# Kernel tuning notes

Hardware: AMD Instinct MI355X
Metric: run time of the kernel (lower is better)

## Reference

```python
import jax, jax.numpy as jnp
import numpy as np

B, P, D, H, DH = 2, 2048, 1024, 16, 64
EPS = 1e-5

def layernorm(x, g, b):
    mu = jnp.mean(x, axis=-1, keepdims=True)
    var = jnp.mean((x - mu) ** 2, axis=-1, keepdims=True)
    return (x - mu) * jax.lax.rsqrt(var + EPS) * g + b

def setup_inputs() -> dict:
    key = jax.random.key(0)
    ks = jax.random.split(key, 16)
    s = lambda *sh: 1.0 / np.sqrt(sh[-2] if len(sh) > 1 else sh[-1])
    return {
        "x": jax.random.normal(ks[0], (B, P, D), jnp.float32),
        "Wq": jax.random.normal(ks[1], (H, D, DH), jnp.float32) / np.sqrt(D),
        "Wk": jax.random.normal(ks[2], (H, D, DH), jnp.float32) / np.sqrt(D),
        "Wv": jax.random.normal(ks[3], (H, D, DH), jnp.float32) / np.sqrt(D),
        "Wp": jax.random.normal(ks[4], (D, D), jnp.float32) / np.sqrt(D),
        "bp": jax.random.normal(ks[5], (D,), jnp.float32) * 0.01,
        "W1": jax.random.normal(ks[6], (D, 4 * D), jnp.float32) / np.sqrt(D),
        "b1": jax.random.normal(ks[7], (4 * D,), jnp.float32) * 0.01,
        "W2": jax.random.normal(ks[8], (4 * D, D), jnp.float32) / np.sqrt(4 * D),
        "b2": jax.random.normal(ks[9], (D,), jnp.float32) * 0.01,
        "g1": jnp.ones((D,), jnp.float32),
        "be1": jnp.zeros((D,), jnp.float32),
        "g2": jnp.ones((D,), jnp.float32),
        "be2": jnp.zeros((D,), jnp.float32),
    }

def reference(x, Wq, Wk, Wv, Wp, bp, W1, b1, W2, b2, g1, be1, g2, be2):
    Bb, Pp, Dd = x.shape
    h = layernorm(x, g1, be1)
    # per-head projections, stacked: [B,H,P,DH]
    q = jnp.einsum('bpd,hde->bhpe', h, Wq)
    k = jnp.einsum('bpd,hde->bhpe', h, Wk)
    v = jnp.einsum('bpd,hde->bhpe', h, Wv)
    # NOTE: source scales by dim_embd**-0.5 (C = x.shape[-1]), not dim_head
    scores = jnp.einsum('bhpe,bhqe->bhpq', q, k) * (Dd ** -0.5)
    mask = jnp.tril(jnp.ones((Pp, Pp), bool))
    scores = jnp.where(mask, scores, -jnp.inf)
    att = jax.nn.softmax(scores, axis=-1)
    o = jnp.einsum('bhpq,bhqe->bhpe', att, v)
    # concat heads: [B,P,H*DH]
    o = o.transpose(0, 2, 1, 3).reshape(Bb, Pp, -1)
    x = x + o @ Wp + bp
    h2 = layernorm(x, g2, be2)
    m = jax.nn.gelu(h2 @ W1 + b1, approximate=False)
    x = x + m @ W2 + b2
    return x
```

## Files before the change

### kernel.cpp

```cpp
#include <hip/hip_runtime.h>
#include <hip/hip_bf16.h>
#include <stdint.h>

typedef unsigned short u16;
typedef __attribute__((ext_vector_type(4))) float f32x4;
typedef __attribute__((ext_vector_type(8))) short bf16x8;
typedef __attribute__((ext_vector_type(4))) short bf16x4;
typedef __attribute__((ext_vector_type(4))) unsigned short u16x4;

static __device__ __forceinline__ u16 f2bf(float f) {
    union { float f; unsigned u; } v; v.f = f;
    unsigned r = v.u + 0x7fffu + ((v.u >> 16) & 1u);
    return (u16)(r >> 16);
}

static __device__ __forceinline__ void gload_lds16(const u16* g, u16* l) {
    __builtin_amdgcn_global_load_lds(
        (const __attribute__((address_space(1))) void*)(uintptr_t)g,
        (__attribute__((address_space(3))) void*)(uint32_t)(uintptr_t)l,
        16, 0, 0);
}

__global__ __launch_bounds__(256) void transpose_cast_b(
    const float* __restrict__ W, u16* __restrict__ out,
    int K, int N, long in_bs, long out_bs)
{
    __shared__ float tile[32][33];
    const float* Wb = W + (size_t)blockIdx.z * in_bs;
    u16* ob = out + (size_t)blockIdx.z * out_bs;
    int nt = blockIdx.x * 32, kt = blockIdx.y * 32;
    int tx = threadIdx.x & 31, ty = threadIdx.x >> 5;
    #pragma unroll
    for (int i = ty; i < 32; i += 8)
        tile[i][tx] = Wb[(size_t)(kt + i) * N + nt + tx];
    __syncthreads();
    #pragma unroll
    for (int i = ty; i < 32; i += 8)
        ob[(size_t)(nt + i) * K + kt + tx] = f2bf(tile[tx][i]);
}

__global__ __launch_bounds__(256) void ln_kernel(
    const float* __restrict__ x, const float* __restrict__ g,
    const float* __restrict__ be, u16* __restrict__ out)
{
    int row = blockIdx.x;
    int t = threadIdx.x;
    const float4* xr = (const float4*)(x + (size_t)row * 1024);
    float4 v = xr[t];
    float s = v.x + v.y + v.z + v.w;
    float sq = v.x * v.x + v.y * v.y + v.z * v.z + v.w * v.w;
    #pragma unroll
    for (int o = 1; o < 64; o <<= 1) {
        s  += __shfl_xor(s, o);
        sq += __shfl_xor(sq, o);
    }
    __shared__ float ps[4], pq[4];
    if ((t & 63) == 0) { ps[t >> 6] = s; pq[t >> 6] = sq; }
    __syncthreads();
    float S = ps[0] + ps[1] + ps[2] + ps[3];
    float Q = pq[0] + pq[1] + pq[2] + pq[3];
    float mu = S * (1.0f / 1024.0f);
    float var = Q * (1.0f / 1024.0f) - mu * mu;
    float rs = rsqrtf(var + 1e-5f);
    const float4 g4  = ((const float4*)g)[t];
    const float4 be4 = ((const float4*)be)[t];
    u16x4 o4;
    o4[0] = f2bf((v.x - mu) * rs * g4.x + be4.x);
    o4[1] = f2bf((v.y - mu) * rs * g4.y + be4.y);
    o4[2] = f2bf((v.z - mu) * rs * g4.z + be4.z);
    o4[3] = f2bf((v.w - mu) * rs * g4.w + be4.w);
    *(u16x4*)(out + (size_t)row * 1024 + t * 4) = o4;
}

template<int EPI>
__global__ __launch_bounds__(256) void gemm_bt(
    const u16* __restrict__ A, const u16* __restrict__ Bt,
    int M, int N, int K,
    const float* __restrict__ bias,
    void* __restrict__ Cout, u16* __restrict__ Kf, u16* __restrict__ Vf)
{
    __shared__ __align__(16) u16 SH[32768];
    const int tm = blockIdx.y * 128, tn = blockIdx.x * 128;
    const int t = threadIdx.x;
    const int lane = t & 63, wave = t >> 6;
    const int wr = wave >> 1, wc = wave & 1;
    const int lq = lane & 15, lg = lane >> 4;
    f32x4 acc[4][4] = {};

    const int srow8 = lane >> 3;
    const int skoff = ((lane & 7) ^ srow8) * 8;
    const u16* ag = A  + (size_t)(tm + wave * 32 + srow8) * K + skoff;
    const u16* bg = Bt + (size_t)(tn + wave * 32 + srow8) * K + skoff;

    auto STAGE = [&](int buf, int k0) {
        u16* ab = SH + buf * 16384 + wave * 2048;
        u16* bb = SH + buf * 16384 + 8192 + wave * 2048;
        #pragma unroll
        for (int j = 0; j < 4; ++j) {
            gload_lds16(ag + (size_t)(j * 8) * K + k0, ab + j * 512);
            gload_lds16(bg + (size_t)(j * 8) * K + k0, bb + j * 512);
        }
    };

    const int KT = K >> 6;
    STAGE(0, 0);
    __syncthreads();
    int buf = 0;
    for (int kt = 0; kt < KT; ++kt) {
        if (kt + 1 < KT) STAGE(buf ^ 1, (kt + 1) << 6);
        const u16* abuf = SH + buf * 16384;
        const u16* bbuf = abuf + 8192;
        bf16x8 af[4][2], bfv[4][2];
        #pragma unroll
        for (int m = 0; m < 4; ++m) {
            const int row = wr * 64 + m * 16 + lq;
            #pragma unroll
            for (int kk = 0; kk < 2; ++kk) {
                const int slot = (kk * 4 + lg) ^ (row & 7);
                af[m][kk] = *(const bf16x8*)(abuf + row * 64 + slot * 8);
            }
        }
        #pragma unroll
        for (int n = 0; n < 4; ++n) {
            const int col = wc * 64 + n * 16 + lq;
            #pragma unroll
            for (int kk = 0; kk < 2; ++kk) {
                const int slot = (kk * 4 + lg) ^ (col & 7);
                bfv[n][kk] = *(const bf16x8*)(bbuf + col * 64 + slot * 8);
            }
        }
        #pragma unroll
        for (int m = 0; m < 4; ++m)
            #pragma unroll
            for (int n = 0; n < 4; ++n)
                #pragma unroll
                for (int kk = 0; kk < 2; ++kk)
                    acc[m][n] = __builtin_amdgcn_mfma_f32_16x16x32_bf16(
                        af[m][kk], bfv[n][kk], acc[m][n], 0, 0, 0);
        __syncthreads();
        buf ^= 1;
    }

    if (EPI == 2 || (EPI == 3 && tn < 1024)) {
        #pragma unroll
        for (int n = 0; n < 4; ++n) {
            const int cl = wc * 64 + n * 16 + lq;
            #pragma unroll
            for (int m = 0; m < 4; ++m) {
                const int rl = wr * 64 + m * 16 + lg * 4;
                #pragma unroll
                for (int r = 0; r < 4; ++r) {
                    float v = acc[m][n][r];
                    if (EPI == 2) {
                        float xx = v + bias[tn + cl];
                        v = 0.5f * xx * (1.0f + erff(xx * 0.70710678118654752f));
                    }
                    SH[(rl + r) * 136 + cl] = f2bf(v);
                }
            }
        }
        __syncthreads();
        const int row = t >> 1, half = t & 1;
        const int ncols = (EPI == 2) ? N : 1024;
        const uint4* srow4 = (const uint4*)(SH + row * 136 + half * 64);
        uint4* drow = (uint4*)((u16*)Cout + (size_t)(tm + row) * ncols + tn + half * 64);
        #pragma unroll
        for (int i = 0; i < 8; ++i)
            drow[i] = srow4[i];
    } else if (EPI == 3) {
        const bool isK = (tn < 2048);
        #pragma unroll
        for (int n = 0; n < 4; ++n) {
            const int cl = wc * 64 + n * 16 + lq;
            const int d = cl & 63, hl = cl >> 6;
            #pragma unroll
            for (int m = 0; m < 4; ++m) {
                const int rl0 = wr * 64 + m * 16 + lg * 4;
                #pragma unroll
                for (int r = 0; r < 4; ++r) {
                    const int rl = rl0 + r;
                    const int p = rl & 63, kl = rl >> 6;
                    int off;
                    if (isK)
                        off = ((p >> 4) * 2 + (d >> 5)) * 512 + ((d >> 3) & 3) * 128
                            + (p & 15) * 8 + (d & 7);
                    else
                        off = ((p >> 4) * 4 + (d >> 4)) * 256 + ((p >> 2) & 3) * 64
                            + (d & 15) * 4 + (p & 3);
                    SH[(hl * 2 + kl) * 4096 + off] = f2bf(acc[m][n][r]);
                }
            }
        }
        __syncthreads();
        const int img = t >> 6, ln = t & 63;
        const int hl = img >> 1, kl = img & 1;
        const int hh = ((tn - (isK ? 1024 : 2048)) >> 6) + hl;
        const int bb = tm >> 11, pp = tm & 2047;
        u16* base = (isK ? Kf : Vf) + (size_t)(bb * 16 + hh) * 131072
                  + (size_t)((pp >> 6) + kl) * 4096;
        const u16* simg = SH + img * 4096;
        #pragma unroll
        for (int i = 0; i < 8; ++i)
            *(uint4*)(base + ln * 8 + i * 512) = *(const uint4*)(simg + ln * 8 + i * 512);
    }
}

__global__ __launch_bounds__(256) void gemm_bt64(
    const u16* __restrict__ A, const u16* __restrict__ Bt,
    int M, int N, int K,
    const float* __restrict__ bias, const float* __restrict__ res,
    float* __restrict__ Cout)
{
    __shared__ __align__(16) u16 As[128 * 32];
    __shared__ __align__(16) u16 Bs[64 * 32];
    const int tm = blockIdx.y * 128, tn = blockIdx.x * 64;
    const int t = threadIdx.x;
    const int lane = t & 63, wave = t >> 6;
    const int wr = wave >> 1, wc = wave & 1;
    const int lq = lane & 15, lg = lane >> 4;
    f32x4 acc[4][2] = {};
    const int srow  = wave * 32 + (lane >> 2);
    const int srowB = wave * 16 + (lane >> 2);
    const int scol = (lane & 3) * 8;
    const u16* ag = A  + (size_t)(tm + srow)  * K + scol;
    const u16* bg = Bt + (size_t)(tn + srowB) * K + scol;
    u16* asl = As + wave * 1024;
    u16* bsl = Bs + wave * 512;
    const size_t rowskip = (size_t)16 * K;
    for (int k0 = 0; k0 < K; k0 += 32) {
        gload_lds16(ag + k0,           asl);
        gload_lds16(ag + k0 + rowskip, asl + 512);
        gload_lds16(bg + k0,           bsl);
        __syncthreads();
        bf16x8 af[4], bfr[2];
        #pragma unroll
        for (int m = 0; m < 4; ++m)
            af[m] = *(const bf16x8*)(As + (wr * 64 + m * 16 + lq) * 32 + lg * 8);
        #pragma unroll
        for (int n = 0; n < 2; ++n)
            bfr[n] = *(const bf16x8*)(Bs + (wc * 32 + n * 16 + lq) * 32 + lg * 8);
        #pragma unroll
        for (int m = 0; m < 4; ++m)
            #pragma unroll
            for (int n = 0; n < 2; ++n)
                acc[m][n] = __builtin_amdgcn_mfma_f32_16x16x32_bf16(af[m], bfr[n], acc[m][n], 0, 0, 0);
        __syncthreads();
    }
    #pragma unroll
    for (int m = 0; m < 4; ++m)
        #pragma unroll
        for (int n = 0; n < 2; ++n) {
            const int col = tn + wc * 32 + n * 16 + lq;
            #pragma unroll
            for (int r = 0; r < 4; ++r) {
                const int row = tm + wr * 64 + m * 16 + lg * 4 + r;
                Cout[(size_t)row * N + col] = acc[m][n][r] + bias[col] + res[(size_t)row * N + col];
            }
        }
}

__global__ __launch_bounds__(256, 4) void attn_kernel(
    const u16* __restrict__ qb, const u16* __restrict__ Kf,
    const u16* __restrict__ Vf, u16* __restrict__ o)
{
    const int P = 2048;
    __shared__ __align__(16) u16 KB[2][4096];
    __shared__ __align__(16) u16 VB[2][4096];
    int blk = blockIdx.x;
    int qt = 31 - (blk >> 5);
    int bh = blk & 31;
    int h = bh & 15, b = bh >> 4;
    int w = threadIdx.x >> 6, lane = threadIdx.x & 63;
    int lq = lane & 15, lg = lane >> 4;
    int q0 = qt * 64 + w * 16;
    const u16* qptr = qb + (size_t)(b * P + q0 + lq) * 1024 + h * 64 + lg * 8;
    bf16x8 qf0 = *(const bf16x8*)qptr;
    bf16x8 qf1 = *(const bf16x8*)(qptr + 32);
    const u16* Kfb = Kf + (size_t)bh * 131072;
    const u16* Vfb = Vf + (size_t)bh * 131072;
    const float C2 = 0.03125f * 1.44269504f;
    const int moff = w * 16 + lq;
    float m2 = -1e30f, l_run = 0.f;
    f32x4 accO[4] = {};
    const int nkvb = qt + 1;

    const int vsel = w >> 1, half = w & 1;
    auto STAGE = [&](int buf, int kvb) {
        const u16* src = (vsel ? Vfb : Kfb) + (size_t)kvb * 4096 + half * 2048 + lane * 8;
        u16* dst = (vsel ? &VB[buf][half * 2048] : &KB[buf][half * 2048]);
        #pragma unroll
        for (int i = 0; i < 4; ++i)
            gload_lds16(src + i * 512, dst + i * 512);
    };

    auto COMPUTE = [&](int buf, bool last) {
        const u16* kbase = KB[buf] + lane * 8;
        f32x4 st[4];
        #pragma unroll
        for (int ss = 0; ss < 4; ++ss) {
            bf16x8 kf0 = *(const bf16x8*)(kbase + ss * 1024);
            bf16x8 kf1 = *(const bf16x8*)(kbase + ss * 1024 + 512);
            f32x4 z = {0.f, 0.f, 0.f, 0.f};
            st[ss] = __builtin_amdgcn_mfma_f32_16x16x32_bf16(kf0, qf0, z, 0, 0, 0);
            st[ss] = __builtin_amdgcn_mfma_f32_16x16x32_bf16(kf1, qf1, st[ss], 0, 0, 0);
        }
        float rmax = -1e30f;
        #pragma unroll
        for (int ss = 0; ss < 4; ++ss)
            #pragma unroll
            for (int r = 0; r < 4; ++r) {
                float v = st[ss][r] * C2;
                if (last && (ss * 16 + lg * 4 + r > moff)) v = -1e30f;
                st[ss][r] = v;
                rmax = fmaxf(rmax, v);
            }
        rmax = fmaxf(rmax, __shfl_xor(rmax, 16));
        rmax = fmaxf(rmax, __shfl_xor(rmax, 32));
        if (__any(rmax > m2 + 11.5f)) {
            float m2n = fmaxf(m2, rmax);
            float alpha = exp2f(m2 - m2n);
            l_run *= alpha;
            #pragma unroll
            for (int r = 0; r < 4; ++r) {
                float ar = __shfl(alpha, lg * 4 + r);
                accO[0][r] *= ar; accO[1][r] *= ar; accO[2][r] *= ar; accO[3][r] *= ar;
            }
            m2 = m2n;
        }
        float psum = 0.f;
        bf16x4 pf[4];
        #pragma unroll
        for (int ss = 0; ss < 4; ++ss)
            #pragma unroll
            for (int r = 0; r < 4; ++r) {
                float pv = exp2f(st[ss][r] - m2);
                psum += pv;
                pf[ss][r] = (short)f2bf(pv);
            }
        psum += __shfl_xor(psum, 16);
        psum += __shfl_xor(psum, 32);
        l_run += psum;
        const u16* vbase = VB[buf] + lane * 4;
        #pragma unroll
        for (int ks = 0; ks < 4; ++ks)
            #pragma unroll
            for (int c = 0; c < 4; ++c) {
                bf16x4 vfr = *(const bf16x4*)(vbase + (ks * 4 + c) * 256);
                accO[c] = __builtin_amdgcn_mfma_f32_16x16x16bf16_1k(pf[ks], vfr, accO[c], 0, 0, 0);
            }
    };

    STAGE(0, 0);
    __syncthreads();
    int cur = 0;
    for (int kvb = 0; kvb < nkvb; ++kvb) {
        if (kvb + 1 < nkvb) STAGE(cur ^ 1, kvb + 1);
        COMPUTE(cur, kvb == nkvb - 1);
        __syncthreads();
        cur ^= 1;
    }

    #pragma unroll
    for (int r = 0; r < 4; ++r) {
        float l_r = __shfl(l_run, lg * 4 + r);
        float inv = 1.0f / l_r;
        size_t orow = (size_t)(b * P + q0 + lg * 4 + r) * 1024 + h * 64;
        #pragma unroll
        for (int c = 0; c < 4; ++c)
            o[orow + c * 16 + lq] = f2bf(accO[c][r] * inv);
    }
}

extern "C" void kernel_launch(void* const* d_in, const int* in_sizes, int n_in,
                              void* d_out, int out_size, void* d_ws, size_t ws_size,
                              hipStream_t stream)
{
    const float* x   = (const float*)d_in[0];
    const float* Wq  = (const float*)d_in[1];
    const float* Wk  = (const float*)d_in[2];
    const float* Wv  = (const float*)d_in[3];
    const float* Wp  = (const float*)d_in[4];
    const float* bp  = (const float*)d_in[5];
    const float* W1  = (const float*)d_in[6];
    const float* b1  = (const float*)d_in[7];
    const float* W2  = (const float*)d_in[8];
    const float* b2  = (const float*)d_in[9];
    const float* g1  = (const float*)d_in[10];
    const float* be1 = (const float*)d_in[11];
    const float* g2  = (const float*)d_in[12];
    const float* be2 = (const float*)d_in[13];

    char* ws = (char*)d_ws;
    u16*  h     = (u16*)(ws + 0);
    u16*  qbuf  = (u16*)(ws + 8388608);
    u16*  Kf    = (u16*)(ws + 16777216);
    u16*  Vf    = (u16*)(ws + 25165824);
    u16*  o     = (u16*)(ws + 33554432);
    float* x1   = (float*)(ws + 41943040);
    u16*  wqkvT = (u16*)(ws + 58720256);
    u16*  wpT   = (u16*)(ws + 65011712);
    u16*  w1T   = (u16*)(ws + 67108864);
    u16*  w2T   = (u16*)(ws + 75497472);
    u16*  m     = (u16*)(ws + 0);
    u16*  h2    = o;
    float* out  = (float*)d_out;

    transpose_cast_b<<<dim3(2, 32, 16), 256, 0, stream>>>(Wq, wqkvT,           1024, 64, 65536, 65536);
    transpose_cast_b<<<dim3(2, 32, 16), 256, 0, stream>>>(Wk, wqkvT + 1048576, 1024, 64, 65536, 65536);
    transpose_cast_b<<<dim3(2, 32, 16), 256, 0, stream>>>(Wv, wqkvT + 2097152, 1024, 64, 65536, 65536);
    transpose_cast_b<<<dim3(32, 32, 1), 256, 0, stream>>>(Wp, wpT, 1024, 1024, 0, 0);
    transpose_cast_b<<<dim3(128, 32, 1), 256, 0, stream>>>(W1, w1T, 1024, 4096, 0, 0);
    transpose_cast_b<<<dim3(32, 128, 1), 256, 0, stream>>>(W2, w2T, 4096, 1024, 0, 0);

    ln_kernel<<<4096, 256, 0, stream>>>(x, g1, be1, h);
    gemm_bt<3><<<dim3(24, 32), 256, 0, stream>>>(h, wqkvT, 4096, 3072, 1024, nullptr, qbuf, Kf, Vf);
    attn_kernel<<<1024, 256, 0, stream>>>(qbuf, Kf, Vf, o);
    gemm_bt64<<<dim3(16, 32), 256, 0, stream>>>(o, wpT, 4096, 1024, 1024, bp, x, x1);
    ln_kernel<<<4096, 256, 0, stream>>>(x1, g2, be2, h2);
    gemm_bt<2><<<dim3(32, 32), 256, 0, stream>>>(h2, w1T, 4096, 4096, 1024, b1, m, nullptr, nullptr);
    gemm_bt64<<<dim3(16, 32), 256, 0, stream>>>(m, w2T, 4096, 1024, 4096, b2, x1, out);
}
```

Measured before the change: 278.2 us.

## Enlarge bf16 GEMM tiles to 256x256 with 512-thread blocks

The QKV and FFN1 GEMMs move from 128x128 tiles with 4 waves to 256x256 tiles with 8 waves, each wave computing 128x64. This doubles the LDS buffer to 128KB and reuses each A fragment across four MFMAs to raise arithmetic intensity per staged byte. The epilogues are rewritten to write the output in two row halves, and the K/V image layout is adapted to the larger tile. It risks lower occupancy (one block per CU), fewer blocks than CUs (192 and 256 blocks), and higher register pressure.

```diff
diff --git a/kernel.cpp b/kernel.cpp
--- a/kernel.cpp
+++ b/kernel.cpp
@@ -73,19 +73,19 @@
 }
 
 template<int EPI>
-__global__ __launch_bounds__(256) void gemm_bt(
+__global__ __launch_bounds__(512, 1) void gemm256(
     const u16* __restrict__ A, const u16* __restrict__ Bt,
     int M, int N, int K,
     const float* __restrict__ bias,
     void* __restrict__ Cout, u16* __restrict__ Kf, u16* __restrict__ Vf)
 {
-    __shared__ __align__(16) u16 SH[32768];
-    const int tm = blockIdx.y * 128, tn = blockIdx.x * 128;
+    __shared__ __align__(16) u16 SH[65536];
+    const int tm = blockIdx.y * 256, tn = blockIdx.x * 256;
     const int t = threadIdx.x;
     const int lane = t & 63, wave = t >> 6;
-    const int wr = wave >> 1, wc = wave & 1;
+    const int wm = wave >> 2, wn = wave & 3;
     const int lq = lane & 15, lg = lane >> 4;
-    f32x4 acc[4][4] = {};
+    f32x4 acc[8][4] = {};
 
     const int srow8 = lane >> 3;
     const int skoff = ((lane & 7) ^ srow8) * 8;
@@ -93,8 +93,8 @@
     const u16* bg = Bt + (size_t)(tn + wave * 32 + srow8) * K + skoff;
 
     auto STAGE = [&](int buf, int k0) {
-        u16* ab = SH + buf * 16384 + wave * 2048;
-        u16* bb = SH + buf * 16384 + 8192 + wave * 2048;
+        u16* ab = SH + buf * 32768 + wave * 2048;
+        u16* bb = SH + buf * 32768 + 16384 + wave * 2048;
         #pragma unroll
         for (int j = 0; j < 4; ++j) {
             gload_lds16(ag + (size_t)(j * 8) * K + k0, ab + j * 512);
@@ -108,21 +108,12 @@
     int buf = 0;
     for (int kt = 0; kt < KT; ++kt) {
         if (kt + 1 < KT) STAGE(buf ^ 1, (kt + 1) << 6);
-        const u16* abuf = SH + buf * 16384;
-        const u16* bbuf = abuf + 8192;
-        bf16x8 af[4][2], bfv[4][2];
-        #pragma unroll
-        for (int m = 0; m < 4; ++m) {
-            const int row = wr * 64 + m * 16 + lq;
-            #pragma unroll
-            for (int kk = 0; kk < 2; ++kk) {
-                const int slot = (kk * 4 + lg) ^ (row & 7);
-                af[m][kk] = *(const bf16x8*)(abuf + row * 64 + slot * 8);
-            }
-        }
+        const u16* abuf = SH + buf * 32768;
+        const u16* bbuf = abuf + 16384;
+        bf16x8 bfv[4][2];
         #pragma unroll
         for (int n = 0; n < 4; ++n) {
-            const int col = wc * 64 + n * 16 + lq;
+            const int col = wn * 64 + n * 16 + lq;
             #pragma unroll
             for (int kk = 0; kk < 2; ++kk) {
                 const int slot = (kk * 4 + lg) ^ (col & 7);
@@ -130,52 +121,62 @@
             }
         }
         #pragma unroll
-        for (int m = 0; m < 4; ++m)
-            #pragma unroll
-            for (int n = 0; n < 4; ++n)
-                #pragma unroll
-                for (int kk = 0; kk < 2; ++kk)
-                    acc[m][n] = __builtin_amdgcn_mfma_f32_16x16x32_bf16(
-                        af[m][kk], bfv[n][kk], acc[m][n], 0, 0, 0);
+        for (int m = 0; m < 8; ++m) {
+            const int row = wm * 128 + m * 16 + lq;
+            const int s0 = lg ^ (row & 7), s1 = (4 + lg) ^ (row & 7);
+            bf16x8 a0 = *(const bf16x8*)(abuf + row * 64 + s0 * 8);
+            bf16x8 a1 = *(const bf16x8*)(abuf + row * 64 + s1 * 8);
+            #pragma unroll
+            for (int n = 0; n < 4; ++n) {
+                acc[m][n] = __builtin_amdgcn_mfma_f32_16x16x32_bf16(a0, bfv[n][0], acc[m][n], 0, 0, 0);
+                acc[m][n] = __builtin_amdgcn_mfma_f32_16x16x32_bf16(a1, bfv[n][1], acc[m][n], 0, 0, 0);
+            }
+        }
         __syncthreads();
         buf ^= 1;
     }
 
     if (EPI == 2 || (EPI == 3 && tn < 1024)) {
-        #pragma unroll
-        for (int n = 0; n < 4; ++n) {
-            const int cl = wc * 64 + n * 16 + lq;
-            #pragma unroll
-            for (int m = 0; m < 4; ++m) {
-                const int rl = wr * 64 + m * 16 + lg * 4;
+        const int ncols = (EPI == 2) ? N : 1024;
+        #pragma unroll
+        for (int rh = 0; rh < 2; ++rh) {
+            if (rh) __syncthreads();
+            if (wm == rh) {
                 #pragma unroll
-                for (int r = 0; r < 4; ++r) {
-                    float v = acc[m][n][r];
-                    if (EPI == 2) {
-                        float xx = v + bias[tn + cl];
-                        v = 0.5f * xx * (1.0f + erff(xx * 0.70710678118654752f));
+                for (int n = 0; n < 4; ++n) {
+                    const int cl = wn * 64 + n * 16 + lq;
+                    #pragma unroll
+                    for (int m = 0; m < 8; ++m) {
+                        const int rl = m * 16 + lg * 4;
+                        #pragma unroll
+                        for (int r = 0; r < 4; ++r) {
+                            float v = acc[m][n][r];
+                            if (EPI == 2) {
+                                float xx = v + bias[tn + cl];
+                                v = 0.5f * xx * (1.0f + erff(xx * 0.70710678118654752f));
+                            }
+                            SH[(rl + r) * 264 + cl] = f2bf(v);
+                        }
                     }
-                    SH[(rl + r) * 136 + cl] = f2bf(v);
                 }
             }
-        }
-        __syncthreads();
-        const int row = t >> 1, half = t & 1;
-        const int ncols = (EPI == 2) ? N : 1024;
-        const uint4* srow4 = (const uint4*)(SH + row * 136 + half * 64);
-        uint4* drow = (uint4*)((u16*)Cout + (size_t)(tm + row) * ncols + tn + half * 64);
-        #pragma unroll
-        for (int i = 0; i < 8; ++i)
-            drow[i] = srow4[i];
+            __syncthreads();
+            const int row = t >> 2, q = t & 3;
+            const uint4* srow4 = (const uint4*)(SH + row * 264 + q * 64);
+            uint4* drow = (uint4*)((u16*)Cout + (size_t)(tm + rh * 128 + row) * ncols + tn + q * 64);
+            #pragma unroll
+            for (int i = 0; i < 8; ++i)
+                drow[i] = srow4[i];
+        }
     } else if (EPI == 3) {
         const bool isK = (tn < 2048);
         #pragma unroll
         for (int n = 0; n < 4; ++n) {
-            const int cl = wc * 64 + n * 16 + lq;
+            const int cl = wn * 64 + n * 16 + lq;
             const int d = cl & 63, hl = cl >> 6;
             #pragma unroll
-            for (int m = 0; m < 4; ++m) {
-                const int rl0 = wr * 64 + m * 16 + lg * 4;
+            for (int m = 0; m < 8; ++m) {
+                const int rl0 = wm * 128 + m * 16 + lg * 4;
                 #pragma unroll
                 for (int r = 0; r < 4; ++r) {
                     const int rl = rl0 + r;
@@ -187,21 +188,21 @@
                     else
                         off = ((p >> 4) * 4 + (d >> 4)) * 256 + ((p >> 2) & 3) * 64
                             + (d & 15) * 4 + (p & 3);
-                    SH[(hl * 2 + kl) * 4096 + off] = f2bf(acc[m][n][r]);
+                    SH[(hl * 4 + kl) * 4096 + off] = f2bf(acc[m][n][r]);
                 }
             }
         }
         __syncthreads();
-        const int img = t >> 6, ln = t & 63;
-        const int hl = img >> 1, kl = img & 1;
+        const int img = t >> 5, ln = t & 31;
+        const int hl = img >> 2, kl = img & 3;
         const int hh = ((tn - (isK ? 1024 : 2048)) >> 6) + hl;
         const int bb = tm >> 11, pp = tm & 2047;
         u16* base = (isK ? Kf : Vf) + (size_t)(bb * 16 + hh) * 131072
                   + (size_t)((pp >> 6) + kl) * 4096;
         const u16* simg = SH + img * 4096;
         #pragma unroll
-        for (int i = 0; i < 8; ++i)
-            *(uint4*)(base + ln * 8 + i * 512) = *(const uint4*)(simg + ln * 8 + i * 512);
+        for (int i = 0; i < 16; ++i)
+            *(uint4*)(base + ln * 8 + i * 256) = *(const uint4*)(simg + ln * 8 + i * 256);
     }
 }
 
@@ -413,10 +414,10 @@
     transpose_cast_b<<<dim3(32, 128, 1), 256, 0, stream>>>(W2, w2T, 4096, 1024, 0, 0);
 
     ln_kernel<<<4096, 256, 0, stream>>>(x, g1, be1, h);
-    gemm_bt<3><<<dim3(24, 32), 256, 0, stream>>>(h, wqkvT, 4096, 3072, 1024, nullptr, qbuf, Kf, Vf);
+    gemm256<3><<<dim3(12, 16), 512, 0, stream>>>(h, wqkvT, 4096, 3072, 1024, nullptr, qbuf, Kf, Vf);
     attn_kernel<<<1024, 256, 0, stream>>>(qbuf, Kf, Vf, o);
     gemm_bt64<<<dim3(16, 32), 256, 0, stream>>>(o, wpT, 4096, 1024, 1024, bp, x, x1);
     ln_kernel<<<4096, 256, 0, stream>>>(x1, g2, be2, h2);
-    gemm_bt<2><<<dim3(32, 32), 256, 0, stream>>>(h2, w1T, 4096, 4096, 1024, b1, m, nullptr, nullptr);
+    gemm256<2><<<dim3(16, 16), 512, 0, stream>>>(h2, w1T, 4096, 4096, 1024, b1, m, nullptr, nullptr);
     gemm_bt64<<<dim3(16, 32), 256, 0, stream>>>(m, w2T, 4096, 1024, 4096, b2, x1, out);
 }
```

New measurement: 418.9 us. +50.6%, slower.
